# Performance work log

Hardware: AMD Instinct MI355X
Metric: run time of the kernel (lower is better)

Reference implementation:

```python
import jax, jax.numpy as jnp
import numpy as np

N, E, G = 50000, 800000, 64          # nodes, edges, graphs in batch
H, C = 4, 32                          # heads, per-head channels
D = H * C                             # 128 = gat_hidden_dim * n_heads
EMB = 16
IN_DIM = 2 * EMB + 1                  # 33
LSTM_H = 256
OUT = 4
V_LAB, V_TYP = 1000, 100
EPS = 1e-5


def _gatv2(x, src, dst, Wl, bl, Wr, br, att, bias):
    # GATv2Conv (PyG semantics, self-loops already appended to src/dst).
    xl = (x @ Wl + bl).reshape(-1, H, C)   # lin_l -> source-side messages x_j
    xr = (x @ Wr + br).reshape(-1, H, C)   # lin_r -> target-side x_i
    xj = xl[src]                            # [Et, H, C]
    e = jax.nn.leaky_relu(xr[dst] + xj, 0.2)
    score = jnp.einsum('ehc,hc->eh', e, att)             # [Et, H]
    smax = jax.ops.segment_max(score, dst, num_segments=N)
    a = jnp.exp(score - smax[dst])
    denom = jax.ops.segment_sum(a, dst, num_segments=N)
    alpha = a / denom[dst]                                # scatter-softmax per dst
    out = jax.ops.segment_sum(xj * alpha[:, :, None], dst, num_segments=N)
    return out.reshape(N, D) + bias


def _graph_norm(x, batch_ids, w, b, ms):
    # PyG GraphNorm: per-graph mean (scaled by learnable ms) and variance.
    cnt = jax.ops.segment_sum(jnp.ones((N,), x.dtype), batch_ids, num_segments=G)[:, None]
    mean = jax.ops.segment_sum(x, batch_ids, num_segments=G) / cnt
    out = x - mean[batch_ids] * ms
    var = jax.ops.segment_sum(out * out, batch_ids, num_segments=G) / cnt
    return w * out / jnp.sqrt(var + EPS)[batch_ids] + b


def _lstm0(x, Wih, Whh, bih, bhh):
    # Single LSTM time-step with h0 = c0 = 0: the Whh @ h0 term vanishes,
    # the forget gate multiplies c0 = 0.  Gate order (PyTorch): i, f, g, o.
    g = x @ Wih.T + bih + bhh
    i, f, gg, o = jnp.split(g, 4, axis=-1)
    c = jax.nn.sigmoid(i) * jnp.tanh(gg)
    return jax.nn.sigmoid(o) * jnp.tanh(c)


def setup_inputs() -> dict:
    key = jax.random.key(0)
    ks = jax.random.split(key, 32)
    rn = lambda k, s, sc=0.05: jax.random.normal(k, s, jnp.float32) * sc
    Z4 = LSTM_H * 4
    return {
        'node_labels': jax.random.randint(ks[0], (N,), 0, V_LAB, jnp.int32),
        'node_types': jax.random.randint(ks[1], (N,), 0, V_TYP, jnp.int32),
        'node_feat': jax.random.normal(ks[2], (N, 1), jnp.float32),
        'edge_index': jax.random.randint(ks[3], (2, E), 0, N, jnp.int32),
        'batch_ids': jnp.sort(jax.random.randint(ks[4], (N,), 0, G, jnp.int32)),
        'emb_label': rn(ks[5], (V_LAB, EMB), 1.0),
        'emb_type': rn(ks[6], (V_TYP, EMB), 1.0),
        'W_in': rn(ks[7], (IN_DIM, D)), 'b_in': jnp.zeros((D,), jnp.float32),
        'g1_Wl': rn(ks[8], (D, D)), 'g1_bl': jnp.zeros((D,), jnp.float32),
        'g1_Wr': rn(ks[9], (D, D)), 'g1_br': jnp.zeros((D,), jnp.float32),
        'g1_att': rn(ks[10], (H, C), 0.1), 'g1_bias': jnp.zeros((D,), jnp.float32),
        'gn1_w': jnp.ones((D,), jnp.float32), 'gn1_b': jnp.zeros((D,), jnp.float32),
        'gn1_ms': jnp.ones((D,), jnp.float32),
        'g2_Wl': rn(ks[11], (D, D)), 'g2_bl': jnp.zeros((D,), jnp.float32),
        'g2_Wr': rn(ks[12], (D, D)), 'g2_br': jnp.zeros((D,), jnp.float32),
        'g2_att': rn(ks[13], (H, C), 0.1), 'g2_bias': jnp.zeros((D,), jnp.float32),
        'gn2_w': jnp.ones((D,), jnp.float32), 'gn2_b': jnp.zeros((D,), jnp.float32),
        'gn2_ms': jnp.ones((D,), jnp.float32),
        'W_res': rn(ks[14], (D, D)), 'b_res': jnp.zeros((D,), jnp.float32),
        'l1_Wih': rn(ks[15], (Z4, D)), 'l1_Whh': rn(ks[16], (Z4, LSTM_H)),
        'l1_bih': jnp.zeros((Z4,), jnp.float32), 'l1_bhh': jnp.zeros((Z4,), jnp.float32),
        'l2_Wih': rn(ks[17], (Z4, LSTM_H)), 'l2_Whh': rn(ks[18], (Z4, LSTM_H)),
        'l2_bih': jnp.zeros((Z4,), jnp.float32), 'l2_bhh': jnp.zeros((Z4,), jnp.float32),
        'ln_w': jnp.ones((LSTM_H,), jnp.float32), 'ln_b': jnp.zeros((LSTM_H,), jnp.float32),
        'fc_W': rn(ks[19], (LSTM_H, OUT)), 'fc_b': jnp.zeros((OUT,), jnp.float32),
    }


def reference(node_labels, node_types, node_feat, edge_index, batch_ids,
              emb_label, emb_type, W_in, b_in,
              g1_Wl, g1_bl, g1_Wr, g1_br, g1_att, g1_bias, gn1_w, gn1_b, gn1_ms,
              g2_Wl, g2_bl, g2_Wr, g2_br, g2_att, g2_bias, gn2_w, gn2_b, gn2_ms,
              W_res, b_res,
              l1_Wih, l1_Whh, l1_bih, l1_bhh, l2_Wih, l2_Whh, l2_bih, l2_bhh,
              ln_w, ln_b, fc_W, fc_b):
    # Node features: [label_emb | type_emb | scalar]  -> [N, 33]
    feat = jnp.concatenate([emb_label[node_labels], emb_type[node_types], node_feat], axis=1)
    # PositionalEncoding at position 0 with odd d_model=33 adds exactly zeros (no-op).
    x = feat @ W_in + b_in                                  # [N, D]

    loops = jnp.arange(N, dtype=edge_index.dtype)           # GATv2Conv add_self_loops=True
    src = jnp.concatenate([edge_index[0], loops])
    dst = jnp.concatenate([edge_index[1], loops])

    x1 = jax.nn.elu(_graph_norm(_gatv2(x, src, dst, g1_Wl, g1_bl, g1_Wr, g1_br, g1_att, g1_bias),
                                batch_ids, gn1_w, gn1_b, gn1_ms))
    # dropout = identity in eval mode
    x2 = jax.nn.elu(_graph_norm(_gatv2(x1, src, dst, g2_Wl, g2_bl, g2_Wr, g2_br, g2_att, g2_bias),
                                batch_ids, gn2_w, gn2_b, gn2_ms) + x1 @ W_res + b_res)

    h1 = _lstm0(x2, l1_Wih, l1_Whh, l1_bih, l1_bhh)         # seq_len = 1 LSTM
    h2 = _lstm0(h1, l2_Wih, l2_Whh, l2_bih, l2_bhh)

    mu = h2.mean(-1, keepdims=True)
    var = ((h2 - mu) ** 2).mean(-1, keepdims=True)
    hn = ln_w * (h2 - mu) / jnp.sqrt(var + EPS) + ln_b      # LayerNorm

    cnt = jax.ops.segment_sum(jnp.ones((N,), hn.dtype), batch_ids, num_segments=G)[:, None]
    pooled = jax.ops.segment_sum(hn, batch_ids, num_segments=G) / cnt  # global_mean_pool
    return jax.nn.log_softmax(pooled @ fc_W + fc_b, axis=1)            # [G, OUT]
```

## Files before the change

kernel.cpp:

```cpp
#include <hip/hip_runtime.h>
#include <cstdint>
#include <cstddef>

#define DD 128
#define LSTMH 256
#define ZG 1024

typedef __attribute__((ext_vector_type(8))) short short8v;
typedef __attribute__((ext_vector_type(4))) float float4v;

static inline int cdiv_(int a, int b) { return (a + b - 1) / b; }

__device__ __forceinline__ float sigm_(float x) { return 1.f / (1.f + __expf(-x)); }
__device__ __forceinline__ float tanh_(float x) {
  float e = __expf(-2.f * fabsf(x));
  float r = (1.f - e) / (1.f + e);
  return copysignf(r, x);
}

__device__ __forceinline__ unsigned short f2bf(float f) {
  uint32_t u = __float_as_uint(f);
  u += 0x7fffu + ((u >> 16) & 1u);
  return (unsigned short)(u >> 16);
}
__device__ __forceinline__ uint32_t bfpack(float a, float b) {
  return (uint32_t)f2bf(a) | ((uint32_t)f2bf(b) << 16);
}
__device__ __forceinline__ float bflo(uint32_t u) { return __uint_as_float(u << 16); }
__device__ __forceinline__ float bfhi(uint32_t u) { return __uint_as_float(u & 0xffff0000u); }

__global__ void prep_all(const float* __restrict__ g1Wl, const float* __restrict__ g1Wr,
                         const float* __restrict__ g2Wl, const float* __restrict__ g2Wr,
                         const float* __restrict__ Wres, const float* __restrict__ l1Wih,
                         const float* __restrict__ l2Wih, const float* __restrict__ g1bl,
                         const float* __restrict__ g1br, const float* __restrict__ g2bl,
                         const float* __restrict__ g2br, const float* __restrict__ bres,
                         const float* __restrict__ l1bih, const float* __restrict__ l1bhh,
                         const float* __restrict__ l2bih, const float* __restrict__ l2bhh,
                         unsigned short* __restrict__ wcat1, unsigned short* __restrict__ wcat2,
                         unsigned short* __restrict__ wl1b, unsigned short* __restrict__ wl2b,
                         float* __restrict__ bcat1, float* __restrict__ bcat2,
                         float* __restrict__ bsum1, float* __restrict__ bsum2,
                         int* __restrict__ deg, int* __restrict__ cursor,
                         float* __restrict__ pooled, int Nn) {
  int i = blockIdx.x * 256 + threadIdx.x;
  if (i < 81920) {
    int seg = i >> 14, j = i & 16383;
    int m = j >> 7, k = j & 127;
    const float* src = (seg == 0) ? g1Wl : (seg == 1) ? g1Wr : (seg == 2) ? g2Wl
                       : (seg == 3) ? g2Wr : Wres;
    unsigned short* dst = (seg == 0) ? wcat1 : (seg == 1) ? wcat1 + 16384
                          : (seg == 2) ? wcat2 : (seg == 3) ? wcat2 + 16384 : wcat2 + 32768;
    dst[j] = f2bf(src[k * 128 + m]);
    return;
  }
  i -= 81920;
  if (i < 131072) { wl1b[i] = f2bf(l1Wih[i]); return; }
  i -= 131072;
  if (i < 262144) { wl2b[i] = f2bf(l2Wih[i]); return; }
  i -= 262144;
  if (i < 256) { bcat1[i] = (i < 128) ? g1bl[i] : g1br[i - 128]; return; }
  i -= 256;
  if (i < 384) {
    bcat2[i] = (i < 128) ? g2bl[i] : (i < 256 ? g2br[i - 128] : bres[i - 256]);
    return;
  }
  i -= 384;
  if (i < 1024) { bsum1[i] = l1bih[i] + l1bhh[i]; return; }
  i -= 1024;
  if (i < 1024) { bsum2[i] = l2bih[i] + l2bhh[i]; return; }
  i -= 1024;
  if (i < Nn) { deg[i] = 0; return; }
  i -= Nn;
  if (i < Nn) { cursor[i] = 0; return; }
  i -= Nn;
  if (i < 16384) { pooled[i] = 0.f; return; }
}

__global__ __launch_bounds__(256) void embed_in2(
    const int* __restrict__ labels, const int* __restrict__ types,
    const float* __restrict__ nf, const float* __restrict__ embL,
    const float* __restrict__ embT, const float* __restrict__ W,
    const float* __restrict__ b, unsigned short* __restrict__ x, int N) {
  __shared__ float f[128][34];
  int base = blockIdx.x * 128;
  int tid = threadIdx.x;
  int ch = tid & 127, half = tid >> 7;
  float wr[33];
#pragma unroll
  for (int k = 0; k < 33; ++k) wr[k] = W[k * 128 + ch];
  float bb = b[ch];
  int nmax = N - base < 128 ? N - base : 128;
  for (int e = tid; e < nmax * 32; e += 256) {
    int n = e >> 5, k = e & 31;
    f[n][k] = (k < 16) ? embL[labels[base + n] * 16 + k] : embT[types[base + n] * 16 + (k - 16)];
  }
  for (int n = tid; n < nmax; n += 256) f[n][32] = nf[base + n];
  __syncthreads();
  for (int n = half; n < nmax; n += 2) {
    float acc = bb;
#pragma unroll
    for (int k = 0; k < 33; ++k) acc = fmaf(f[n][k], wr[k], acc);
    x[(size_t)(base + n) * 128 + ch] = f2bf(acc);
  }
}

__global__ void count_deg(const int* __restrict__ ei, int* __restrict__ deg, int E_, int N_) {
  int i = blockIdx.x * 256 + threadIdx.x;
  if (i < E_) atomicAdd(&deg[ei[E_ + i]], 1);
  else if (i < E_ + N_) atomicAdd(&deg[i - E_], 1);
}

__global__ __launch_bounds__(256) void scan1(const int* __restrict__ deg, int* __restrict__ offs,
                                             int* __restrict__ partials, int N_) {
  __shared__ int buf[2][256];
  int tid = threadIdx.x;
  int i = blockIdx.x * 256 + tid;
  int v = (i < N_) ? deg[i] : 0;
  buf[0][tid] = v;
  __syncthreads();
  int cur = 0;
#pragma unroll
  for (int d = 1; d < 256; d <<= 1) {
    int xv = buf[cur][tid];
    if (tid >= d) xv += buf[cur][tid - d];
    buf[cur ^ 1][tid] = xv;
    cur ^= 1;
    __syncthreads();
  }
  int incl = buf[cur][tid];
  if (i < N_) offs[i] = incl - v;
  if (tid == 255) partials[blockIdx.x] = incl;
}

__global__ __launch_bounds__(256) void scan2(int* __restrict__ partials, int* __restrict__ offs,
                                             int nb, int N_) {
  __shared__ int buf[2][256];
  int tid = threadIdx.x;
  int v = (tid < nb) ? partials[tid] : 0;
  buf[0][tid] = v;
  __syncthreads();
  int cur = 0;
#pragma unroll
  for (int d = 1; d < 256; d <<= 1) {
    int xv = buf[cur][tid];
    if (tid >= d) xv += buf[cur][tid - d];
    buf[cur ^ 1][tid] = xv;
    cur ^= 1;
    __syncthreads();
  }
  int incl = buf[cur][tid];
  if (tid < nb) partials[tid] = incl - v;
  if (tid == 255) offs[N_] = incl;
}

__global__ void scan3(int* __restrict__ offs, const int* __restrict__ partials, int N_) {
  int i = blockIdx.x * 256 + threadIdx.x;
  if (i < N_) offs[i] += partials[blockIdx.x];
}

__global__ void fill_csr(const int* __restrict__ ei, const int* __restrict__ offs,
                         int* __restrict__ cursor, int* __restrict__ csr, int E_, int N_) {
  int i = blockIdx.x * 256 + threadIdx.x;
  int s, d;
  if (i < E_) { s = ei[i]; d = ei[E_ + i]; }
  else if (i < E_ + N_) { s = d = i - E_; }
  else return;
  int pos = offs[d] + atomicAdd(&cursor[d], 1);
  csr[pos] = s;
}

__global__ void graph_ranges(const int* __restrict__ bids, int* __restrict__ gstart,
                             float* __restrict__ invcnt, int N_, int G_) {
  int t = threadIdx.x;
  if (t <= G_) {
    int lo = 0, hi = N_;
    while (lo < hi) { int mid = (lo + hi) >> 1; if (bids[mid] < t) lo = mid + 1; else hi = mid; }
    gstart[t] = lo;
  }
  __syncthreads();
  if (t < G_) {
    int c = gstart[t + 1] - gstart[t];
    invcnt[t] = (c > 0) ? 1.f / (float)c : 0.f;
  }
}

__global__ __launch_bounds__(256) void gemm_bf16(
    const unsigned short* __restrict__ A, const unsigned short* __restrict__ Bp,
    const float* __restrict__ bias, unsigned short* __restrict__ C, int M, int K, int Ncols) {
  __shared__ unsigned short As[128 * 40];
  __shared__ unsigned short Bs[128 * 40];
  int tid = threadIdx.x;
  int lane = tid & 63;
  int wid = tid >> 6;
  int rowBase = blockIdx.y * 128, colBase = blockIdx.x * 128;
  int wr = (wid >> 1) * 64, wc = (wid & 1) * 64;
  int fr = lane & 15, fg = lane >> 4;
  float4v acc[4][4];
#pragma unroll
  for (int i = 0; i < 4; ++i)
#pragma unroll
    for (int j = 0; j < 4; ++j) acc[i][j] = (float4v){0.f, 0.f, 0.f, 0.f};

  int sr = tid >> 2;
  int sc = tid & 3;
  int off_lo = (sc < 2) ? 32 * sc : 32 * sc - 56;

  for (int k0 = 0; k0 < K; k0 += 32) {
#pragma unroll
    for (int it = 0; it < 2; ++it) {
      int r = it * 64 + sr;
      uint4 va = make_uint4(0u, 0u, 0u, 0u);
      if (rowBase + r < M)
        va = *(const uint4*)(A + (size_t)(rowBase + r) * K + k0 + sc * 8);
      char* arow = (char*)(As + r * 40);
      *(uint2*)(arow + off_lo) = make_uint2(va.x, va.y);
      *(uint2*)(arow + off_lo + 16) = make_uint2(va.z, va.w);
      uint4 vb = *(const uint4*)(Bp + (size_t)(colBase + r) * K + k0 + sc * 8);
      char* brow = (char*)(Bs + r * 40);
      *(uint2*)(brow + off_lo) = make_uint2(vb.x, vb.y);
      *(uint2*)(brow + off_lo + 16) = make_uint2(vb.z, vb.w);
    }
    __syncthreads();
    short8v af[4], bfv[4];
#pragma unroll
    for (int i = 0; i < 4; ++i)
      af[i] = *(const short8v*)((const char*)As + (wr + 16 * i + fr) * 80 + fg * 16);
#pragma unroll
    for (int j = 0; j < 4; ++j)
      bfv[j] = *(const short8v*)((const char*)Bs + (wc + 16 * j + fr) * 80 + fg * 16);
#pragma unroll
    for (int i = 0; i < 4; ++i)
#pragma unroll
      for (int j = 0; j < 4; ++j)
        acc[i][j] = __builtin_amdgcn_mfma_f32_16x16x32_bf16(af[i], bfv[j], acc[i][j], 0, 0, 0);
    __syncthreads();
  }
#pragma unroll
  for (int j = 0; j < 4; ++j) {
    int gc = colBase + wc + 16 * j + fr;
    float bv = bias[gc];
#pragma unroll
    for (int i = 0; i < 4; ++i) {
      int gr0 = rowBase + wr + 16 * i + fg * 4;
#pragma unroll
      for (int rg = 0; rg < 4; ++rg) {
        int gr = gr0 + rg;
        if (gr < M) C[(size_t)gr * Ncols + gc] = f2bf(acc[i][j][rg] + bv);
      }
    }
  }
}

__global__ __launch_bounds__(256) void gat_agg(
    const unsigned short* __restrict__ xlr, int stride,
    const int* __restrict__ csr, const int* __restrict__ offs,
    const float* __restrict__ att, const float* __restrict__ bias,
    unsigned short* __restrict__ out, float* __restrict__ gz, int N) {
  int zt = blockIdx.x * 256 + threadIdx.x;
  if (zt < 4096) *(float4*)(gz + zt * 4) = make_float4(0.f, 0.f, 0.f, 0.f);
  int wid = zt >> 6;
  if (wid >= N) return;
  int lane = threadIdx.x & 63;
  int q = lane >> 4, ql = lane & 15;
  float4 aA = *(const float4*)&att[ql * 8];
  float4 aB = *(const float4*)&att[ql * 8 + 4];
  uint4 ur = *(const uint4*)(xlr + (size_t)wid * stride + 128 + ql * 8);
  float r0 = bflo(ur.x), r1 = bfhi(ur.x), r2 = bflo(ur.y), r3 = bfhi(ur.y);
  float r4 = bflo(ur.z), r5 = bfhi(ur.z), r6 = bflo(ur.w), r7 = bfhi(ur.w);
  float m = -1e30f, L = 0.f;
  float s0 = 0.f, s1 = 0.f, s2 = 0.f, s3 = 0.f, s4 = 0.f, s5 = 0.f, s6 = 0.f, s7 = 0.f;
  int js = offs[wid], je = offs[wid + 1];
  for (int j = js + q; j < je; j += 4) {
    int s = csr[j];
    uint4 u = *(const uint4*)(xlr + (size_t)s * stride + ql * 8);
    float x0 = bflo(u.x), x1 = bfhi(u.x), x2 = bflo(u.y), x3 = bfhi(u.y);
    float x4 = bflo(u.z), x5 = bfhi(u.z), x6 = bflo(u.w), x7 = bfhi(u.w);
    float v0 = fmaxf(r0 + x0, 0.2f * (r0 + x0));
    float v1 = fmaxf(r1 + x1, 0.2f * (r1 + x1));
    float v2 = fmaxf(r2 + x2, 0.2f * (r2 + x2));
    float v3 = fmaxf(r3 + x3, 0.2f * (r3 + x3));
    float v4 = fmaxf(r4 + x4, 0.2f * (r4 + x4));
    float v5 = fmaxf(r5 + x5, 0.2f * (r5 + x5));
    float v6 = fmaxf(r6 + x6, 0.2f * (r6 + x6));
    float v7 = fmaxf(r7 + x7, 0.2f * (r7 + x7));
    float p = aA.x * v0 + aA.y * v1 + aA.z * v2 + aA.w * v3 +
              aB.x * v4 + aB.y * v5 + aB.z * v6 + aB.w * v7;
    p += __shfl_xor(p, 1); p += __shfl_xor(p, 2);
    float mn = fmaxf(m, p);
    float ea = __expf(p - mn);
    float es = __expf(m - mn);
    L = L * es + ea;
    s0 = s0 * es + ea * x0; s1 = s1 * es + ea * x1;
    s2 = s2 * es + ea * x2; s3 = s3 * es + ea * x3;
    s4 = s4 * es + ea * x4; s5 = s5 * es + ea * x5;
    s6 = s6 * es + ea * x6; s7 = s7 * es + ea * x7;
    m = mn;
  }
#pragma unroll
  for (int d = 16; d <= 32; d <<= 1) {
    float mo = __shfl_xor(m, d), Lo = __shfl_xor(L, d);
    float t0 = __shfl_xor(s0, d), t1 = __shfl_xor(s1, d);
    float t2 = __shfl_xor(s2, d), t3 = __shfl_xor(s3, d);
    float t4 = __shfl_xor(s4, d), t5 = __shfl_xor(s5, d);
    float t6 = __shfl_xor(s6, d), t7 = __shfl_xor(s7, d);
    float mn = fmaxf(m, mo);
    float e0 = __expf(m - mn), e1 = __expf(mo - mn);
    L = L * e0 + Lo * e1;
    s0 = s0 * e0 + t0 * e1; s1 = s1 * e0 + t1 * e1;
    s2 = s2 * e0 + t2 * e1; s3 = s3 * e0 + t3 * e1;
    s4 = s4 * e0 + t4 * e1; s5 = s5 * e0 + t5 * e1;
    s6 = s6 * e0 + t6 * e1; s7 = s7 * e0 + t7 * e1;
    m = mn;
  }
  if (q == 0) {
    float inv = 1.f / L;
    float4 bA = *(const float4*)&bias[ql * 8];
    float4 bB = *(const float4*)&bias[ql * 8 + 4];
    uint4 ov;
    ov.x = bfpack(s0 * inv + bA.x, s1 * inv + bA.y);
    ov.y = bfpack(s2 * inv + bA.z, s3 * inv + bA.w);
    ov.z = bfpack(s4 * inv + bB.x, s5 * inv + bB.y);
    ov.w = bfpack(s6 * inv + bB.z, s7 * inv + bB.w);
    *(uint4*)(out + (size_t)wid * DD + ql * 8) = ov;
  }
}

__global__ __launch_bounds__(256) void gn_stats2(const unsigned short* __restrict__ x,
                                                 const int* __restrict__ bids,
                                                 float* __restrict__ gsum,
                                                 float* __restrict__ gsq, int N) {
  int base = blockIdx.x * 128;
  int cp = threadIdx.x & 63;
  int sub = threadIdx.x >> 6;
  int end = base + 128 < N ? base + 128 : N;
  int curg = -1;
  float s0 = 0.f, s1 = 0.f, q0 = 0.f, q1 = 0.f;
  for (int r = base + sub; r < end; r += 4) {
    int g = bids[r];
    if (g != curg) {
      if (curg >= 0) {
        atomicAdd(&gsum[curg * DD + cp * 2], s0);
        atomicAdd(&gsum[curg * DD + cp * 2 + 1], s1);
        atomicAdd(&gsq[curg * DD + cp * 2], q0);
        atomicAdd(&gsq[curg * DD + cp * 2 + 1], q1);
      }
      curg = g; s0 = s1 = q0 = q1 = 0.f;
    }
    uint32_t u = *(const uint32_t*)(x + (size_t)r * DD + cp * 2);
    float v0 = bflo(u), v1 = bfhi(u);
    s0 += v0; q0 += v0 * v0; s1 += v1; q1 += v1 * v1;
  }
  if (curg >= 0) {
    atomicAdd(&gsum[curg * DD + cp * 2], s0);
    atomicAdd(&gsum[curg * DD + cp * 2 + 1], s1);
    atomicAdd(&gsq[curg * DD + cp * 2], q0);
    atomicAdd(&gsq[curg * DD + cp * 2 + 1], q1);
  }
}

template <bool ADDRES>
__global__ void gn_apply(const unsigned short* __restrict__ xin,
                         unsigned short* __restrict__ xout,
                         const unsigned short* __restrict__ res, int resStride,
                         const int* __restrict__ bids, const float* __restrict__ gsum,
                         const float* __restrict__ gsq, const float* __restrict__ invcnt,
                         const float* __restrict__ w, const float* __restrict__ b,
                         const float* __restrict__ ms, int N) {
  int idx = blockIdx.x * 256 + threadIdx.x;
  if (idx >= N * 64) return;
  int n = idx >> 6, cp = idx & 63;
  int g = bids[n];
  float ic = invcnt[g];
  float2 sm = *(const float2*)&gsum[g * DD + cp * 2];
  float2 sq = *(const float2*)&gsq[g * DD + cp * 2];
  float2 w2 = *(const float2*)&w[cp * 2];
  float2 b2 = *(const float2*)&b[cp * 2];
  float2 m2 = *(const float2*)&ms[cp * 2];
  uint32_t u = *(const uint32_t*)(xin + (size_t)n * DD + cp * 2);
  float mean0 = sm.x * ic, mean1 = sm.y * ic;
  float mm0 = mean0 * m2.x, mm1 = mean1 * m2.y;
  float var0 = sq.x * ic - mm0 * (2.f * mean0 - mm0);
  float var1 = sq.y * ic - mm1 * (2.f * mean1 - mm1);
  float v0 = (bflo(u) - mm0) * rsqrtf(var0 + 1e-5f) * w2.x + b2.x;
  float v1 = (bfhi(u) - mm1) * rsqrtf(var1 + 1e-5f) * w2.y + b2.y;
  if (ADDRES) {
    uint32_t ur = *(const uint32_t*)(res + (size_t)n * resStride + cp * 2);
    v0 += bflo(ur); v1 += bfhi(ur);
  }
  v0 = v0 > 0.f ? v0 : (__expf(v0) - 1.f);
  v1 = v1 > 0.f ? v1 : (__expf(v1) - 1.f);
  *(uint32_t*)(xout + (size_t)n * DD + cp * 2) = bfpack(v0, v1);
}

template <int KD>
__global__ __launch_bounds__(256, 4) void lstm_big(
    const unsigned short* __restrict__ A, const unsigned short* __restrict__ Bp,
    const float* __restrict__ bsum, unsigned short* __restrict__ H, int M) {
  __shared__ __attribute__((aligned(16))) char As_[128 * 136];
  __shared__ __attribute__((aligned(16))) char Ws_[96 * 136];
  const int NPH = KD / 64;
  int npanel = (M + 127) >> 7;
  int b = blockIdx.x;
  int g8 = b & 7, inner = b >> 3;
  int p = g8 + 8 * (inner >> 3);
  int cc = inner & 7;
  if (p >= npanel) return;
  int rowBase = p << 7;
  int ch0 = cc * 32;

  int tid = threadIdx.x;
  int lane = tid & 63;
  int wid = tid >> 6;
  int wr2 = wid >> 1;
  int wc2 = wid & 1;
  int fr = lane & 15, fg = lane >> 4;

  int aldst[4], agoff[4];
  bool aval[4];
#pragma unroll
  for (int q = 0; q < 4; ++q) {
    int e = q * 256 + tid;
    int r = e >> 3, kk = e & 7;
    int c = kk >> 2, sc = kk & 3;
    int olo = (sc < 2) ? 32 * sc : 32 * sc - 56;
    aldst[q] = r * 136 + c * 64 + olo;
    aval[q] = (rowBase + r) < M;
    agoff[q] = (rowBase + r) * KD + c * 32 + sc * 8;
  }
  int wldst[3], wgoff[3];
#pragma unroll
  for (int q = 0; q < 3; ++q) {
    int e = q * 256 + tid;
    int wrow = e >> 3, kk = e & 7;
    int c = kk >> 2, sc = kk & 3;
    int half = wrow >= 48 ? 1 : 0;
    int r3 = wrow - 48 * half;
    int grp = r3 >> 4;
    int goff = (grp == 0) ? 0 : (grp == 1 ? 512 : 768);
    int grow = goff + ch0 + 16 * half + (r3 & 15);
    int olo = (sc < 2) ? 32 * sc : 32 * sc - 56;
    wldst[q] = wrow * 136 + c * 64 + olo;
    wgoff[q] = grow * KD + c * 32 + sc * 8;
  }

  float4v acc[4][3];
#pragma unroll
  for (int i = 0; i < 4; ++i)
#pragma unroll
    for (int j = 0; j < 3; ++j) acc[i][j] = (float4v){0.f, 0.f, 0.f, 0.f};

  uint4 va[4], vw[3];
#pragma unroll
  for (int q = 0; q < 4; ++q) {
    va[q] = make_uint4(0u, 0u, 0u, 0u);
    if (aval[q]) va[q] = *(const uint4*)(A + agoff[q]);
  }
#pragma unroll
  for (int q = 0; q < 3; ++q) vw[q] = *(const uint4*)(Bp + wgoff[q]);

#pragma unroll
  for (int ph = 0; ph < NPH; ++ph) {
    if (ph) __syncthreads();
#pragma unroll
    for (int q = 0; q < 4; ++q) {
      char* dst = As_ + aldst[q];
      *(uint2*)(dst) = make_uint2(va[q].x, va[q].y);
      *(uint2*)(dst + 16) = make_uint2(va[q].z, va[q].w);
    }
#pragma unroll
    for (int q = 0; q < 3; ++q) {
      char* dst = Ws_ + wldst[q];
      *(uint2*)(dst) = make_uint2(vw[q].x, vw[q].y);
      *(uint2*)(dst + 16) = make_uint2(vw[q].z, vw[q].w);
    }
    __syncthreads();
    if (ph + 1 < NPH) {
      int koff = (ph + 1) * 64;
#pragma unroll
      for (int q = 0; q < 4; ++q) {
        va[q] = make_uint4(0u, 0u, 0u, 0u);
        if (aval[q]) va[q] = *(const uint4*)(A + agoff[q] + koff);
      }
#pragma unroll
      for (int q = 0; q < 3; ++q) vw[q] = *(const uint4*)(Bp + wgoff[q] + koff);
    }
    __builtin_amdgcn_s_setprio(1);
#pragma unroll
    for (int c = 0; c < 2; ++c) {
      short8v af[4], bf[3];
#pragma unroll
      for (int i = 0; i < 4; ++i)
        af[i] = *(const short8v*)(As_ + (64 * wr2 + 16 * i + fr) * 136 + c * 64 + fg * 16);
#pragma unroll
      for (int j = 0; j < 3; ++j)
        bf[j] = *(const short8v*)(Ws_ + (48 * wc2 + 16 * j + fr) * 136 + c * 64 + fg * 16);
#pragma unroll
      for (int i = 0; i < 4; ++i)
#pragma unroll
        for (int j = 0; j < 3; ++j)
          acc[i][j] = __builtin_amdgcn_mfma_f32_16x16x32_bf16(af[i], bf[j], acc[i][j], 0, 0, 0);
    }
    __builtin_amdgcn_s_setprio(0);
  }
  int chL = 16 * wc2 + fr;
  int ch = ch0 + chL;
  float bi = bsum[ch], bg = bsum[512 + ch], bo = bsum[768 + ch];
  unsigned short hv[16];
#pragma unroll
  for (int i = 0; i < 4; ++i) {
#pragma unroll
    for (int rg = 0; rg < 4; ++rg) {
      float iv = acc[i][0][rg] + bi;
      float gv = acc[i][1][rg] + bg;
      float ov = acc[i][2][rg] + bo;
      float c = sigm_(iv) * tanh_(gv);
      hv[i * 4 + rg] = f2bf(sigm_(ov) * tanh_(c));
    }
  }
  __syncthreads();
  unsigned short* Hs = (unsigned short*)As_;
#pragma unroll
  for (int i = 0; i < 4; ++i) {
#pragma unroll
    for (int rg = 0; rg < 4; ++rg) {
      int row = 64 * wr2 + 16 * i + 4 * fg + rg;
      Hs[row * 40 + chL] = hv[i * 4 + rg];
    }
  }
  __syncthreads();
#pragma unroll
  for (int q = 0; q < 2; ++q) {
    int e = q * 256 + tid;
    int row = e >> 2, seg = e & 3;
    if (rowBase + row < M) {
      uint4 v = *(const uint4*)(Hs + row * 40 + seg * 8);
      *(uint4*)(H + (size_t)(rowBase + row) * LSTMH + ch0 + seg * 8) = v;
    }
  }
}

__global__ __launch_bounds__(256) void ln_pool2(
    const unsigned short* __restrict__ h2, const int* __restrict__ bids,
    const float* __restrict__ lnw, const float* __restrict__ lnb,
    const float* __restrict__ invcnt, float* __restrict__ pooled, int N) {
  int wave = (blockIdx.x * 256 + threadIdx.x) >> 6;
  int lane = threadIdx.x & 63;
  int r0 = wave * 8;
  if (r0 >= N) return;
  float4 w4 = *(const float4*)&lnw[lane * 4];
  float4 b4 = *(const float4*)&lnb[lane * 4];
  float p0 = 0.f, p1 = 0.f, p2 = 0.f, p3 = 0.f;
  int curg = bids[r0];
  int rend = r0 + 8 < N ? r0 + 8 : N;
  for (int r = r0; r < rend; ++r) {
    int g = bids[r];
    if (g != curg) {
      float ic = invcnt[curg];
      atomicAdd(&pooled[curg * LSTMH + lane * 4 + 0], p0 * ic);
      atomicAdd(&pooled[curg * LSTMH + lane * 4 + 1], p1 * ic);
      atomicAdd(&pooled[curg * LSTMH + lane * 4 + 2], p2 * ic);
      atomicAdd(&pooled[curg * LSTMH + lane * 4 + 3], p3 * ic);
      p0 = p1 = p2 = p3 = 0.f;
      curg = g;
    }
    uint2 u = *(const uint2*)(h2 + (size_t)r * LSTMH + lane * 4);
    float v0 = bflo(u.x), v1 = bfhi(u.x), v2 = bflo(u.y), v3 = bfhi(u.y);
    float s = v0 + v1 + v2 + v3;
    float q = v0 * v0 + v1 * v1 + v2 * v2 + v3 * v3;
#pragma unroll
    for (int d = 1; d < 64; d <<= 1) { s += __shfl_xor(s, d); q += __shfl_xor(q, d); }
    float mu = s * (1.f / 256.f);
    float var = q * (1.f / 256.f) - mu * mu;
    float rs = rsqrtf(var + 1e-5f);
    p0 += w4.x * (v0 - mu) * rs + b4.x;
    p1 += w4.y * (v1 - mu) * rs + b4.y;
    p2 += w4.z * (v2 - mu) * rs + b4.z;
    p3 += w4.w * (v3 - mu) * rs + b4.w;
  }
  float ic = invcnt[curg];
  atomicAdd(&pooled[curg * LSTMH + lane * 4 + 0], p0 * ic);
  atomicAdd(&pooled[curg * LSTMH + lane * 4 + 1], p1 * ic);
  atomicAdd(&pooled[curg * LSTMH + lane * 4 + 2], p2 * ic);
  atomicAdd(&pooled[curg * LSTMH + lane * 4 + 3], p3 * ic);
}

__global__ __launch_bounds__(64) void fc_lsm(const float* __restrict__ pooled,
                                             const float* __restrict__ W,
                                             const float* __restrict__ b, float* __restrict__ out) {
  int g = blockIdx.x;
  int t = threadIdx.x;
  float l0 = 0.f, l1 = 0.f, l2 = 0.f, l3 = 0.f;
  for (int k = t; k < LSTMH; k += 64) {
    float p = pooled[g * LSTMH + k];
    l0 += p * W[k * 4 + 0];
    l1 += p * W[k * 4 + 1];
    l2 += p * W[k * 4 + 2];
    l3 += p * W[k * 4 + 3];
  }
#pragma unroll
  for (int d = 1; d < 64; d <<= 1) {
    l0 += __shfl_xor(l0, d); l1 += __shfl_xor(l1, d);
    l2 += __shfl_xor(l2, d); l3 += __shfl_xor(l3, d);
  }
  if (t == 0) {
    float z[4] = {l0 + b[0], l1 + b[1], l2 + b[2], l3 + b[3]};
    float mx = fmaxf(fmaxf(z[0], z[1]), fmaxf(z[2], z[3]));
    float sum = __expf(z[0] - mx) + __expf(z[1] - mx) + __expf(z[2] - mx) + __expf(z[3] - mx);
    float ls = logf(sum);
#pragma unroll
    for (int o = 0; o < 4; ++o) out[g * 4 + o] = z[o] - mx - ls;
  }
}

extern "C" void kernel_launch(void* const* d_in, const int* in_sizes, int n_in,
                              void* d_out, int out_size, void* d_ws, size_t ws_size,
                              hipStream_t stream) {
  const int* node_labels = (const int*)d_in[0];
  const int* node_types = (const int*)d_in[1];
  const float* node_feat = (const float*)d_in[2];
  const int* edge_index = (const int*)d_in[3];
  const int* batch_ids = (const int*)d_in[4];
  const float* emb_label = (const float*)d_in[5];
  const float* emb_type = (const float*)d_in[6];
  const float* W_in = (const float*)d_in[7];
  const float* b_in = (const float*)d_in[8];
  const float* g1_Wl = (const float*)d_in[9];
  const float* g1_bl = (const float*)d_in[10];
  const float* g1_Wr = (const float*)d_in[11];
  const float* g1_br = (const float*)d_in[12];
  const float* g1_att = (const float*)d_in[13];
  const float* g1_bias = (const float*)d_in[14];
  const float* gn1_w = (const float*)d_in[15];
  const float* gn1_b = (const float*)d_in[16];
  const float* gn1_ms = (const float*)d_in[17];
  const float* g2_Wl = (const float*)d_in[18];
  const float* g2_bl = (const float*)d_in[19];
  const float* g2_Wr = (const float*)d_in[20];
  const float* g2_br = (const float*)d_in[21];
  const float* g2_att = (const float*)d_in[22];
  const float* g2_bias = (const float*)d_in[23];
  const float* gn2_w = (const float*)d_in[24];
  const float* gn2_b = (const float*)d_in[25];
  const float* gn2_ms = (const float*)d_in[26];
  const float* W_res = (const float*)d_in[27];
  const float* b_res = (const float*)d_in[28];
  const float* l1_Wih = (const float*)d_in[29];
  const float* l1_bih = (const float*)d_in[31];
  const float* l1_bhh = (const float*)d_in[32];
  const float* l2_Wih = (const float*)d_in[33];
  const float* l2_bih = (const float*)d_in[35];
  const float* l2_bhh = (const float*)d_in[36];
  const float* ln_w = (const float*)d_in[37];
  const float* ln_b = (const float*)d_in[38];
  const float* fc_W = (const float*)d_in[39];
  const float* fc_b = (const float*)d_in[40];
  float* out = (float*)d_out;

  const int N = in_sizes[0];
  const int E = in_sizes[3] / 2;
  const int G = out_size / 4;
  const int ET = E + N;

  char* wsb = (char*)d_ws;
  size_t off = 0;
  auto alloc = [&](size_t bytes) -> void* {
    void* p = (void*)(wsb + off);
    off = (off + bytes + 255) & ~(size_t)255;
    return p;
  };
  unsigned short* xA = (unsigned short*)alloc((size_t)N * 512);
  unsigned short* xb = (unsigned short*)alloc((size_t)N * DD * 2);
  unsigned short* xlr = (unsigned short*)alloc((size_t)N * 384 * 2);
  int* deg = (int*)alloc((size_t)N * 4);
  int* offs = (int*)alloc((size_t)(N + 1) * 4);
  int* cursor = (int*)alloc((size_t)N * 4);
  int* partials = (int*)alloc(1024);
  int* csr = (int*)alloc((size_t)ET * 4);
  int* gstart = (int*)alloc((size_t)(G + 1) * 4);
  float* invcnt = (float*)alloc((size_t)G * 4);
  float* gsum = (float*)alloc((size_t)G * DD * 4);
  float* gsq = (float*)alloc((size_t)G * DD * 4);
  float* pooled = (float*)alloc((size_t)G * LSTMH * 4);
  float* bcat1 = (float*)alloc(256 * 4);
  float* bcat2 = (float*)alloc(384 * 4);
  float* bsum1 = (float*)alloc(ZG * 4);
  float* bsum2 = (float*)alloc(ZG * 4);
  unsigned short* wcat1 = (unsigned short*)alloc((size_t)256 * DD * 2);
  unsigned short* wcat2 = (unsigned short*)alloc((size_t)384 * DD * 2);
  unsigned short* wl1b = (unsigned short*)alloc((size_t)ZG * DD * 2);
  unsigned short* wl2b = (unsigned short*)alloc((size_t)ZG * LSTMH * 2);
  (void)ws_size; (void)n_in;

  unsigned short* h1 = xlr;
  unsigned short* h2 = xA;

  int prepTotal = 477824 + 2 * N + 16384;
  prep_all<<<cdiv_(prepTotal, 256), 256, 0, stream>>>(
      g1_Wl, g1_Wr, g2_Wl, g2_Wr, W_res, l1_Wih, l2_Wih,
      g1_bl, g1_br, g2_bl, g2_br, b_res, l1_bih, l1_bhh, l2_bih, l2_bhh,
      wcat1, wcat2, wl1b, wl2b, bcat1, bcat2, bsum1, bsum2,
      deg, cursor, pooled, N);
  graph_ranges<<<1, 128, 0, stream>>>(batch_ids, gstart, invcnt, N, G);
  embed_in2<<<cdiv_(N, 128), 256, 0, stream>>>(node_labels, node_types, node_feat, emb_label,
                                               emb_type, W_in, b_in, xb, N);

  count_deg<<<cdiv_(ET, 256), 256, 0, stream>>>(edge_index, deg, E, N);
  int nb1 = cdiv_(N, 256);
  scan1<<<nb1, 256, 0, stream>>>(deg, offs, partials, N);
  scan2<<<1, 256, 0, stream>>>(partials, offs, nb1, N);
  scan3<<<nb1, 256, 0, stream>>>(offs, partials, N);
  fill_csr<<<cdiv_(ET, 256), 256, 0, stream>>>(edge_index, offs, cursor, csr, E, N);

  int mb = cdiv_(N, 128);
  gemm_bf16<<<dim3(2, mb), 256, 0, stream>>>(xb, wcat1, bcat1, xlr, N, DD, 256);
  gat_agg<<<cdiv_(N, 4), 256, 0, stream>>>(xlr, 256, csr, offs, g1_att, g1_bias, xA, gsum, N);
  gn_stats2<<<cdiv_(N, 128), 256, 0, stream>>>(xA, batch_ids, gsum, gsq, N);
  gn_apply<false><<<cdiv_(N * 64, 256), 256, 0, stream>>>(
      xA, xb, nullptr, 0, batch_ids, gsum, gsq, invcnt, gn1_w, gn1_b, gn1_ms, N);
  gemm_bf16<<<dim3(3, mb), 256, 0, stream>>>(xb, wcat2, bcat2, xlr, N, DD, 384);
  gat_agg<<<cdiv_(N, 4), 256, 0, stream>>>(xlr, 384, csr, offs, g2_att, g2_bias, xA, gsum, N);
  gn_stats2<<<cdiv_(N, 128), 256, 0, stream>>>(xA, batch_ids, gsum, gsq, N);
  gn_apply<true><<<cdiv_(N * 64, 256), 256, 0, stream>>>(
      xA, xb, xlr + 256, 384, batch_ids, gsum, gsq, invcnt, gn2_w, gn2_b, gn2_ms, N);
  int npanel = cdiv_(N, 128);
  int lblocks = 64 * cdiv_(npanel, 8);
  lstm_big<DD><<<lblocks, 256, 0, stream>>>(xb, wl1b, bsum1, h1, N);
  lstm_big<LSTMH><<<lblocks, 256, 0, stream>>>(h1, wl2b, bsum2, h2, N);
  ln_pool2<<<cdiv_(N, 32), 256, 0, stream>>>(h2, batch_ids, ln_w, ln_b, invcnt, pooled, N);
  fc_lsm<<<G, 64, 0, stream>>>(pooled, fc_W, fc_b, out);
}
```

Baseline: 470.3 us.

## Load LSTM GEMM MFMA fragments directly from global memory, dropping LDS staging

The LSTM gate GEMM stops staging the A and weight tiles through shared memory with barriers. Each lane now reads its bf16 MFMA fragments straight from global memory, relying on L1/L2 caching for reuse across waves. This removes LDS writes, LDS reads and the per-phase __syncthreads, and shrinks LDS to the small output staging buffer, which may allow more blocks per CU. In exchange, loads are now strided row fragments rather than coalesced tile loads. The row bounds check on A is gone, so the last partial panel can read past the end of the buffer.

```diff
diff --git a/kernel.cpp b/kernel.cpp
--- a/kernel.cpp
+++ b/kernel.cpp
@@ -397,9 +397,7 @@
 __global__ __launch_bounds__(256, 4) void lstm_big(
     const unsigned short* __restrict__ A, const unsigned short* __restrict__ Bp,
     const float* __restrict__ bsum, unsigned short* __restrict__ H, int M) {
-  __shared__ __attribute__((aligned(16))) char As_[128 * 136];
-  __shared__ __attribute__((aligned(16))) char Ws_[96 * 136];
-  const int NPH = KD / 64;
+  __shared__ unsigned short Hs[128 * 40];
   int npanel = (M + 127) >> 7;
   int b = blockIdx.x;
   int g8 = b & 7, inner = b >> 3;
@@ -416,33 +414,11 @@
   int wc2 = wid & 1;
   int fr = lane & 15, fg = lane >> 4;
 
-  int aldst[4], agoff[4];
-  bool aval[4];
-#pragma unroll
-  for (int q = 0; q < 4; ++q) {
-    int e = q * 256 + tid;
-    int r = e >> 3, kk = e & 7;
-    int c = kk >> 2, sc = kk & 3;
-    int olo = (sc < 2) ? 32 * sc : 32 * sc - 56;
-    aldst[q] = r * 136 + c * 64 + olo;
-    aval[q] = (rowBase + r) < M;
-    agoff[q] = (rowBase + r) * KD + c * 32 + sc * 8;
-  }
-  int wldst[3], wgoff[3];
-#pragma unroll
-  for (int q = 0; q < 3; ++q) {
-    int e = q * 256 + tid;
-    int wrow = e >> 3, kk = e & 7;
-    int c = kk >> 2, sc = kk & 3;
-    int half = wrow >= 48 ? 1 : 0;
-    int r3 = wrow - 48 * half;
-    int grp = r3 >> 4;
-    int goff = (grp == 0) ? 0 : (grp == 1 ? 512 : 768);
-    int grow = goff + ch0 + 16 * half + (r3 & 15);
-    int olo = (sc < 2) ? 32 * sc : 32 * sc - 56;
-    wldst[q] = wrow * 136 + c * 64 + olo;
-    wgoff[q] = grow * KD + c * 32 + sc * 8;
-  }
+  const unsigned short* abase = A + (size_t)(rowBase + 64 * wr2 + fr) * KD + fg * 8;
+  int wrow = ch0 + 16 * wc2 + fr;
+  const unsigned short* wb0 = Bp + (size_t)(wrow) * KD + fg * 8;
+  const unsigned short* wb1 = Bp + (size_t)(512 + wrow) * KD + fg * 8;
+  const unsigned short* wb2 = Bp + (size_t)(768 + wrow) * KD + fg * 8;
 
   float4v acc[4][3];
 #pragma unroll
@@ -450,63 +426,24 @@
 #pragma unroll
     for (int j = 0; j < 3; ++j) acc[i][j] = (float4v){0.f, 0.f, 0.f, 0.f};
 
-  uint4 va[4], vw[3];
-#pragma unroll
-  for (int q = 0; q < 4; ++q) {
-    va[q] = make_uint4(0u, 0u, 0u, 0u);
-    if (aval[q]) va[q] = *(const uint4*)(A + agoff[q]);
-  }
-#pragma unroll
-  for (int q = 0; q < 3; ++q) vw[q] = *(const uint4*)(Bp + wgoff[q]);
-
-#pragma unroll
-  for (int ph = 0; ph < NPH; ++ph) {
-    if (ph) __syncthreads();
-#pragma unroll
-    for (int q = 0; q < 4; ++q) {
-      char* dst = As_ + aldst[q];
-      *(uint2*)(dst) = make_uint2(va[q].x, va[q].y);
-      *(uint2*)(dst + 16) = make_uint2(va[q].z, va[q].w);
-    }
-#pragma unroll
-    for (int q = 0; q < 3; ++q) {
-      char* dst = Ws_ + wldst[q];
-      *(uint2*)(dst) = make_uint2(vw[q].x, vw[q].y);
-      *(uint2*)(dst + 16) = make_uint2(vw[q].z, vw[q].w);
-    }
-    __syncthreads();
-    if (ph + 1 < NPH) {
-      int koff = (ph + 1) * 64;
-#pragma unroll
-      for (int q = 0; q < 4; ++q) {
-        va[q] = make_uint4(0u, 0u, 0u, 0u);
-        if (aval[q]) va[q] = *(const uint4*)(A + agoff[q] + koff);
-      }
-#pragma unroll
-      for (int q = 0; q < 3; ++q) vw[q] = *(const uint4*)(Bp + wgoff[q] + koff);
-    }
-    __builtin_amdgcn_s_setprio(1);
-#pragma unroll
-    for (int c = 0; c < 2; ++c) {
-      short8v af[4], bf[3];
-#pragma unroll
-      for (int i = 0; i < 4; ++i)
-        af[i] = *(const short8v*)(As_ + (64 * wr2 + 16 * i + fr) * 136 + c * 64 + fg * 16);
+#pragma unroll
+  for (int k0 = 0; k0 < KD; k0 += 32) {
+    short8v af[4], bf[3];
+#pragma unroll
+    for (int i = 0; i < 4; ++i)
+      af[i] = *(const short8v*)(abase + (size_t)(16 * i) * KD + k0);
+    bf[0] = *(const short8v*)(wb0 + k0);
+    bf[1] = *(const short8v*)(wb1 + k0);
+    bf[2] = *(const short8v*)(wb2 + k0);
+#pragma unroll
+    for (int i = 0; i < 4; ++i)
 #pragma unroll
       for (int j = 0; j < 3; ++j)
-        bf[j] = *(const short8v*)(Ws_ + (48 * wc2 + 16 * j + fr) * 136 + c * 64 + fg * 16);
-#pragma unroll
-      for (int i = 0; i < 4; ++i)
-#pragma unroll
-        for (int j = 0; j < 3; ++j)
-          acc[i][j] = __builtin_amdgcn_mfma_f32_16x16x32_bf16(af[i], bf[j], acc[i][j], 0, 0, 0);
-    }
-    __builtin_amdgcn_s_setprio(0);
+        acc[i][j] = __builtin_amdgcn_mfma_f32_16x16x32_bf16(af[i], bf[j], acc[i][j], 0, 0, 0);
   }
   int chL = 16 * wc2 + fr;
   int ch = ch0 + chL;
   float bi = bsum[ch], bg = bsum[512 + ch], bo = bsum[768 + ch];
-  unsigned short hv[16];
 #pragma unroll
   for (int i = 0; i < 4; ++i) {
 #pragma unroll
@@ -515,17 +452,8 @@
       float gv = acc[i][1][rg] + bg;
       float ov = acc[i][2][rg] + bo;
       float c = sigm_(iv) * tanh_(gv);
-      hv[i * 4 + rg] = f2bf(sigm_(ov) * tanh_(c));
-    }
-  }
-  __syncthreads();
-  unsigned short* Hs = (unsigned short*)As_;
-#pragma unroll
-  for (int i = 0; i < 4; ++i) {
-#pragma unroll
-    for (int rg = 0; rg < 4; ++rg) {
       int row = 64 * wr2 + 16 * i + 4 * fg + rg;
-      Hs[row * 40 + chL] = hv[i * 4 + rg];
+      Hs[row * 40 + chL] = f2bf(sigm_(ov) * tanh_(c));
     }
   }
   __syncthreads();
```

New measurement: 515.6 us. 9.7% more time.
